# Performance work log

Hardware: AMD Instinct MI355X
Metric: run time of the kernel (lower is better)

Reference implementation:

```python
import jax, jax.numpy as jnp
import numpy as np

VOCAB = 64
TEMPERATURE = 0.1


def one_hot_argmax(x, temperature):
    """Straight-through one-hot argmax (edward2 disc_utils.one_hot_argmax)."""
    hard = jax.nn.one_hot(jnp.argmax(x, axis=-1), x.shape[-1], dtype=x.dtype)
    soft = jax.nn.softmax(x / temperature, axis=-1)
    return soft + jax.lax.stop_gradient(hard - soft)


def one_hot_add(inputs, shift):
    """(inputs + shift) % V in one-hot space = circular convolution via FFT."""
    out = jnp.fft.ifft(jnp.fft.fft(inputs) * jnp.fft.fft(shift))
    return jnp.real(out).astype(inputs.dtype)


def one_hot_multiply(inputs, scale):
    """(inputs * scale) % V in one-hot space.

    out[..., u] = sum_{c>=1, v} scale[..., c] * inputs[..., v] * [(c*v) % V == u]
    (edward2 zeroes the c==0 row). Implemented as a scan over the V scale
    values with a scatter-add along the vocab axis: O(B*L*V) memory, no
    [B, L, V, V] intermediate.
    """
    V = inputs.shape[-1]
    c_idx = jnp.arange(V)
    mult_idx = (c_idx[:, None] * c_idx[None, :]) % V          # [c, v] -> (c*v)%V
    scale_c = jnp.moveaxis(scale, -1, 0)                      # [V, B, L]
    mask = (c_idx != 0).astype(inputs.dtype)                  # zero the c=0 row

    def step(acc, xs):
        idx_c, sc, m = xs                                     # [V], [B, L], []
        contrib = jnp.zeros_like(inputs).at[..., idx_c].add(inputs)
        return acc + (m * sc)[..., None] * contrib, None

    out, _ = jax.lax.scan(step, jnp.zeros_like(inputs), (mult_idx, scale_c, mask))
    return out


def setup_inputs() -> dict:
    key = jax.random.key(0)
    k1, k2 = jax.random.split(key, 2)
    B, L, V = 16, 8192, VOCAB
    labels = jax.random.randint(k1, (B, L), 0, V)
    inputs = jax.nn.one_hot(labels, V, dtype=jnp.float32)     # [B, L, V] one-hot
    W = jax.random.normal(k2, (V, 2 * V), dtype=jnp.float32) * 0.02
    b = jnp.zeros((2 * V,), dtype=jnp.float32)
    return {"inputs": inputs, "W": W, "b": b}


def reference(inputs, W, b):
    """DiscreteAutoregressiveFlow.forward (data -> latent, parallel pass)."""
    V = inputs.shape[-1]
    net = inputs @ W + b                                      # [B, L, 2V]
    loc, scale = net[..., :V], net[..., V:]
    scale = one_hot_argmax(scale, TEMPERATURE).astype(inputs.dtype)
    scaled_inputs = one_hot_multiply(inputs, scale)
    loc = one_hot_argmax(loc, TEMPERATURE).astype(inputs.dtype)
    return one_hot_add(scaled_inputs, loc)
```

## Files before the change

### kernel.cpp

```cpp
#include <hip/hip_runtime.h>

#define VOC 64
#define CHUNKS 8
#define TPB 256

__global__ __launch_bounds__(TPB) void flow_fused_kernel(
    const float* __restrict__ in,
    const float* __restrict__ W,
    const float* __restrict__ b,
    float* __restrict__ out,
    int n_chunks)
{
    __shared__ int s_lut[VOC];

    const int tid = threadIdx.x;
    const size_t base = (size_t)blockIdx.x * (TPB * CHUNKS) + tid;
    const float4* in4  = reinterpret_cast<const float4*>(in);
    float4*       out4 = reinterpret_cast<float4*>(out);

    const int v = tid >> 2;
    const int q = tid & 3;
    const float4* rowL = reinterpret_cast<const float4*>(W + v * 2 * VOC) + q * 4;
    const float4* rowS = rowL + (VOC / 4);
    const float4* b4   = reinterpret_cast<const float4*>(b);

    float4 wL[4], wS[4], bL[4], bS[4];
    #pragma unroll
    for (int k = 0; k < 4; ++k) {
        wL[k] = rowL[k];
        wS[k] = rowS[k];
        bL[k] = b4[q * 4 + k];
        bS[k] = b4[16 + q * 4 + k];
    }

    float4 vin[CHUNKS];
    #pragma unroll
    for (int i = 0; i < CHUNKS; ++i) {
        size_t c = base + (size_t)i * TPB;
        if (c < (size_t)n_chunks) vin[i] = in4[c];
        else                      vin[i] = make_float4(0.f, 0.f, 0.f, 0.f);
    }

    {
        float bvL = -3.402823466e+38f; int biL = 0;
        float bvS = -3.402823466e+38f; int biS = 0;
        #pragma unroll
        for (int k = 0; k < 4; ++k) {
            float x0 = wL[k].x + bL[k].x, x1 = wL[k].y + bL[k].y;
            float x2 = wL[k].z + bL[k].z, x3 = wL[k].w + bL[k].w;
            float y0 = wS[k].x + bS[k].x, y1 = wS[k].y + bS[k].y;
            float y2 = wS[k].z + bS[k].z, y3 = wS[k].w + bS[k].w;
            int ib = q * 16 + k * 4;
            if (x0 > bvL) { bvL = x0; biL = ib;     }
            if (x1 > bvL) { bvL = x1; biL = ib + 1; }
            if (x2 > bvL) { bvL = x2; biL = ib + 2; }
            if (x3 > bvL) { bvL = x3; biL = ib + 3; }
            if (y0 > bvS) { bvS = y0; biS = ib;     }
            if (y1 > bvS) { bvS = y1; biS = ib + 1; }
            if (y2 > bvS) { bvS = y2; biS = ib + 2; }
            if (y3 > bvS) { bvS = y3; biS = ib + 3; }
        }
        #pragma unroll
        for (int off = 1; off < 4; off <<= 1) {
            float ov = __shfl_xor(bvL, off, 4);
            int   oi = __shfl_xor(biL, off, 4);
            if (ov > bvL || (ov == bvL && oi < biL)) { bvL = ov; biL = oi; }
            ov = __shfl_xor(bvS, off, 4);
            oi = __shfl_xor(biS, off, 4);
            if (ov > bvS || (ov == bvS && oi < biS)) { bvS = ov; biS = oi; }
        }
        if (q == 0) s_lut[v] = (biS == 0) ? -1 : (biS * v + biL) % VOC;
    }
    __syncthreads();

    const int lane = tid & 63;
    const int grp  = lane >> 4;
    const int gb   = lane & ~15;
    const int sub  = tid & 15;
    const int b4i  = sub << 2;

    #pragma unroll
    for (int i = 0; i < CHUNKS; ++i) {
        size_t c = base + (size_t)i * TPB;
        float4 x = vin[i];
        int li = -1;
        if (x.x > 0.5f) li = 0;
        if (x.y > 0.5f) li = 1;
        if (x.z > 0.5f) li = 2;
        if (x.w > 0.5f) li = 3;
        unsigned long long m = __ballot(li >= 0);
        unsigned gm = (unsigned)((m >> (grp * 16)) & 0xFFFFull);
        if (gm == 0) continue;
        int wlane = __builtin_ctz(gm);
        int lw    = __shfl(li, gb + wlane, 64);
        int bi    = (wlane << 2) + lw;

        int oidx = s_lut[bi];

        float4 vo;
        vo.x = (oidx == b4i)     ? 1.0f : 0.0f;
        vo.y = (oidx == b4i + 1) ? 1.0f : 0.0f;
        vo.z = (oidx == b4i + 2) ? 1.0f : 0.0f;
        vo.w = (oidx == b4i + 3) ? 1.0f : 0.0f;
        if (c < (size_t)n_chunks)
            out4[c] = vo;
    }
}

extern "C" void kernel_launch(void* const* d_in, const int* in_sizes, int n_in,
                              void* d_out, int out_size, void* d_ws, size_t ws_size,
                              hipStream_t stream) {
    const float* inputs = (const float*)d_in[0];
    const float* W      = (const float*)d_in[1];
    const float* b      = (const float*)d_in[2];
    float* out = (float*)d_out;

    int n_rows   = in_sizes[0] / VOC;
    int n_chunks = n_rows * 16;

    int per_block = TPB * CHUNKS;
    int blocks = (n_chunks + per_block - 1) / per_block;

    flow_fused_kernel<<<blocks, TPB, 0, stream>>>(inputs, W, b, out, n_chunks);
}
```

Measured before the change: 18.46 us.

## Use nontemporal loads/stores, ballot-based index decode, and 512-thread blocks

Doubles the block size to 512 threads, and only the first 256 threads compute the per-vocab lookup table. Input and output now use nontemporal vector loads and stores to skip cache pollution on streaming data. The cross-lane shuffle that recovered the hot index is replaced by two extra ballots that decode the within-chunk position bits. A row with no hot bit now writes zeros instead of skipping the store. The larger block halves the grid and raises per-block LUT setup latency relative to work.

Measured after the change: 17.11 us. 1.08x faster.

```diff
diff --git a/kernel.cpp b/kernel.cpp
--- a/kernel.cpp
+++ b/kernel.cpp
@@ -2,7 +2,9 @@
 
 #define VOC 64
 #define CHUNKS 8
-#define TPB 256
+#define TPB 512
+
+typedef float f32x4 __attribute__((ext_vector_type(4)));
 
 __global__ __launch_bounds__(TPB) void flow_fused_kernel(
     const float* __restrict__ in,
@@ -15,33 +17,34 @@
 
     const int tid = threadIdx.x;
     const size_t base = (size_t)blockIdx.x * (TPB * CHUNKS) + tid;
-    const float4* in4  = reinterpret_cast<const float4*>(in);
-    float4*       out4 = reinterpret_cast<float4*>(out);
+    const f32x4* in4  = reinterpret_cast<const f32x4*>(in);
+    f32x4*       out4 = reinterpret_cast<f32x4*>(out);
 
+    f32x4 wL[4], wS[4], bL[4], bS[4];
     const int v = tid >> 2;
     const int q = tid & 3;
-    const float4* rowL = reinterpret_cast<const float4*>(W + v * 2 * VOC) + q * 4;
-    const float4* rowS = rowL + (VOC / 4);
-    const float4* b4   = reinterpret_cast<const float4*>(b);
-
-    float4 wL[4], wS[4], bL[4], bS[4];
-    #pragma unroll
-    for (int k = 0; k < 4; ++k) {
-        wL[k] = rowL[k];
-        wS[k] = rowS[k];
-        bL[k] = b4[q * 4 + k];
-        bS[k] = b4[16 + q * 4 + k];
+    if (tid < 256) {
+        const f32x4* rowL = reinterpret_cast<const f32x4*>(W + v * 2 * VOC) + q * 4;
+        const f32x4* rowS = rowL + (VOC / 4);
+        const f32x4* b4   = reinterpret_cast<const f32x4*>(b);
+        #pragma unroll
+        for (int k = 0; k < 4; ++k) {
+            wL[k] = rowL[k];
+            wS[k] = rowS[k];
+            bL[k] = b4[q * 4 + k];
+            bS[k] = b4[16 + q * 4 + k];
+        }
     }
 
-    float4 vin[CHUNKS];
+    f32x4 vin[CHUNKS];
     #pragma unroll
     for (int i = 0; i < CHUNKS; ++i) {
         size_t c = base + (size_t)i * TPB;
-        if (c < (size_t)n_chunks) vin[i] = in4[c];
-        else                      vin[i] = make_float4(0.f, 0.f, 0.f, 0.f);
+        if (c < (size_t)n_chunks) vin[i] = __builtin_nontemporal_load(&in4[c]);
+        else                      vin[i] = (f32x4){0.f, 0.f, 0.f, 0.f};
     }
 
-    {
+    if (tid < 256) {
         float bvL = -3.402823466e+38f; int biL = 0;
         float bvS = -3.402823466e+38f; int biS = 0;
         #pragma unroll
@@ -75,35 +78,41 @@
 
     const int lane = tid & 63;
     const int grp  = lane >> 4;
-    const int gb   = lane & ~15;
     const int sub  = tid & 15;
     const int b4i  = sub << 2;
 
     #pragma unroll
     for (int i = 0; i < CHUNKS; ++i) {
         size_t c = base + (size_t)i * TPB;
-        float4 x = vin[i];
+        f32x4 x = vin[i];
         int li = -1;
         if (x.x > 0.5f) li = 0;
         if (x.y > 0.5f) li = 1;
         if (x.z > 0.5f) li = 2;
         if (x.w > 0.5f) li = 3;
-        unsigned long long m = __ballot(li >= 0);
-        unsigned gm = (unsigned)((m >> (grp * 16)) & 0xFFFFull);
-        if (gm == 0) continue;
-        int wlane = __builtin_ctz(gm);
-        int lw    = __shfl(li, gb + wlane, 64);
-        int bi    = (wlane << 2) + lw;
+        unsigned long long mh = __ballot(li >= 0);
+        unsigned long long m0 = __ballot(li >= 0 && (li & 1));
+        unsigned long long m1 = __ballot(li >= 2);
 
-        int oidx = s_lut[bi];
+        unsigned gmh = (unsigned)((mh >> (grp * 16)) & 0xFFFFull);
+        int oidx;
+        if (gmh == 0) {
+            oidx = -1;
+        } else {
+            int wl   = __builtin_ctz(gmh);
+            int wbit = grp * 16 + wl;
+            int liw  = (int)((m0 >> wbit) & 1ull) | ((int)((m1 >> wbit) & 1ull) << 1);
+            int bi   = (wl << 2) | liw;
+            oidx = s_lut[bi];
+        }
 
-        float4 vo;
+        f32x4 vo;
         vo.x = (oidx == b4i)     ? 1.0f : 0.0f;
         vo.y = (oidx == b4i + 1) ? 1.0f : 0.0f;
         vo.z = (oidx == b4i + 2) ? 1.0f : 0.0f;
         vo.w = (oidx == b4i + 3) ? 1.0f : 0.0f;
         if (c < (size_t)n_chunks)
-            out4[c] = vo;
+            __builtin_nontemporal_store(vo, &out4[c]);
     }
 }
 
```
